# Kernel tuning notes

Measured on AMD Instinct MI355X. Metric: run time of the kernel, lower is better.

The kernel has to match this reference:

```python
import jax, jax.numpy as jnp
import numpy as np

B = 8                                   # point clouds per batch
NS = [65536, 16384, 4096, 1024, 256]    # points per scale (stride-4 downsampling)
CS = [32, 64, 128, 256, 512]            # encoder channels per scale
K = 3
BN_EPS = 1e-5


def setup_inputs() -> dict:
    key = jax.random.key(0)
    ks = iter(jax.random.split(key, 64))
    inp = {}
    for i, (n, c) in enumerate(zip(NS, CS)):
        inp[f"p{i}"] = jax.random.uniform(next(ks), (n, 3), jnp.float32)
        inp[f"f{i}"] = jax.random.normal(next(ks), (n, c), jnp.float32)
        inp[f"b{i}"] = jnp.repeat(jnp.arange(B, dtype=jnp.int32), n // B)
    # FP stage mlps: a:(4->3) [768,256,256], b:(3->2) [384,128,128],
    #               c:(2->1) [192,64,64],   d:(1->0) [96,32,32]
    cfg = {"a": (CS[3] + CS[4], CS[3]), "b": (CS[2] + CS[3], CS[2]),
           "c": (CS[1] + CS[2], CS[1]), "d": (CS[0] + CS[1], CS[0])}
    for s, (cin, ch) in cfg.items():
        for j, ci in ((1, cin), (2, ch)):
            inp[f"w{s}{j}"] = jax.random.normal(next(ks), (ci, ch), jnp.float32) / float(np.sqrt(ci))
            inp[f"bias{s}{j}"] = jnp.zeros((ch,), jnp.float32)
            inp[f"g{s}{j}"] = jnp.ones((ch,), jnp.float32)
            inp[f"bt{s}{j}"] = jnp.zeros((ch,), jnp.float32)
    return inp


def _knn_interpolate(x2, p2, p1):
    """torch_geometric.nn.knn_interpolate with k=3; equal-sized sorted batches."""
    n1, n2, c = p1.shape[0] // B, p2.shape[0] // B, x2.shape[1]
    p1b, p2b = p1.reshape(B, n1, 3), p2.reshape(B, n2, 3)
    x2b = x2.reshape(B, n2, c)
    # squared dists via |a|^2 + |b|^2 - 2ab (avoids [B,n1,n2,3] temporary)
    d2 = (jnp.sum(p1b * p1b, -1)[:, :, None] + jnp.sum(p2b * p2b, -1)[:, None, :]
          - 2.0 * jnp.einsum('bnd,bmd->bnm', p1b, p2b))
    neg_d2, idx = jax.lax.top_k(-d2, K)              # [B, n1, K]
    w = 1.0 / jnp.maximum(-neg_d2, 1e-16)            # inverse squared distance
    gath = jax.vmap(lambda x, i: x[i])(x2b, idx)     # [B, n1, K, c]
    out = jnp.einsum('bnk,bnkc->bnc', w, gath) / jnp.sum(w, -1, keepdims=True)
    return out.reshape(B * n1, c)


def _lin_bn_relu(x, w, bias, gamma, beta):
    h = x @ w + bias
    mu = jnp.mean(h, 0)
    var = jnp.mean((h - mu) ** 2, 0)
    return jax.nn.relu((h - mu) * jax.lax.rsqrt(var + BN_EPS) * gamma + beta)


def _fp_stage(p_fine, f_fine, p_coarse, f_coarse, w1, b1, g1, bt1, w2, b2, g2, bt2):
    up = _knn_interpolate(f_coarse, p_coarse, p_fine)
    x = jnp.concatenate([f_fine, up], axis=1)
    x = _lin_bn_relu(x, w1, b1, g1, bt1)
    return _lin_bn_relu(x, w2, b2, g2, bt2)


def reference(p0, p1, p2, p3, p4, f0, f1, f2, f3, f4, b0, b1, b2, b3, b4,
              wa1, biasa1, ga1, bta1, wa2, biasa2, ga2, bta2,
              wb1, biasb1, gb1, btb1, wb2, biasb2, gb2, btb2,
              wc1, biasc1, gc1, btc1, wc2, biasc2, gc2, btc2,
              wd1, biasd1, gd1, btd1, wd2, biasd2, gd2, btd2):
    f3 = _fp_stage(p3, f3, p4, f4, wa1, biasa1, ga1, bta1, wa2, biasa2, ga2, bta2)
    f2 = _fp_stage(p2, f2, p3, f3, wb1, biasb1, gb1, btb1, wb2, biasb2, gb2, btb2)
    f1 = _fp_stage(p1, f1, p2, f2, wc1, biasc1, gc1, btc1, wc2, biasc2, gc2, btc2)
    f0 = _fp_stage(p0, f0, p1, f1, wd1, biasd1, gd1, btd1, wd2, biasd2, gd2, btd2)
    return f0
```

## Files before the change

### kernel.cpp

```cpp
#include <hip/hip_runtime.h>

#define BN_EPS 1e-5f

typedef unsigned short us;

__device__ __forceinline__ float bf2f(us u) {
    union { unsigned int i; float f; } v; v.i = ((unsigned int)u) << 16; return v.f;
}
__device__ __forceinline__ us f2bf(float f) {
    unsigned int x = __float_as_uint(f);
    x += 0x7fffu + ((x >> 16) & 1u);
    return (us)(x >> 16);
}
__device__ __forceinline__ float ldf(const void* p, size_t i, int f32) {
    return f32 ? ((const float*)p)[i] : bf2f(((const us*)p)[i]);
}

__global__ void detect_kernel(const unsigned int* __restrict__ g, int* __restrict__ flag) {
    if (threadIdx.x == 0 && blockIdx.x == 0)
        *flag = ((g[0] & 0xFFFFu) == 0u) ? 1 : 0;
}

__global__ __launch_bounds__(256)
void prep_aos_kernel(const void* __restrict__ p, float4* __restrict__ aos,
                     const int* __restrict__ pf32, int n)
{
    const int i = blockIdx.x * 256 + threadIdx.x;
    if (i >= n) return;
    const int f32 = *pf32;
    const float x = ldf(p, (size_t)3 * i + 0, f32);
    const float y = ldf(p, (size_t)3 * i + 1, f32);
    const float z = ldf(p, (size_t)3 * i + 2, f32);
    const float s2 = __fadd_rn(__fadd_rn(__fmul_rn(x, x), __fmul_rn(y, y)), __fmul_rn(z, z));
    aos[i] = make_float4(__fadd_rn(x, x), __fadd_rn(y, y), __fadd_rn(z, z), s2);
}

__device__ __forceinline__ void lexmerge33(
    const float a0, const int A0, const float a1, const int A1, const float a2, const int A2,
    const float b0, const int B0, const float b1, const int B1, const float b2, const int B2,
    float& m0, int& M0, float& m1, int& M1, float& m2, int& M2)
{
    const bool c1 = (a0 < b0) || (a0 == b0 && A0 < B0);
    m0 = c1 ? a0 : b0;  M0 = c1 ? A0 : B0;
    const float hAd = c1 ? a1 : a0;  const int hAi = c1 ? A1 : A0;
    const float hBd = c1 ? b0 : b1;  const int hBi = c1 ? B0 : B1;
    const bool c2 = (hAd < hBd) || (hAd == hBd && hAi < hBi);
    m1 = c2 ? hAd : hBd;  M1 = c2 ? hAi : hBi;
    const float gAd = c2 ? (c1 ? a2 : a1) : hAd;  const int gAi = c2 ? (c1 ? A2 : A1) : hAi;
    const float gBd = c2 ? hBd : (c1 ? b1 : b2);  const int gBi = c2 ? hBi : (c1 ? B1 : B2);
    const bool c3 = (gAd < gBd) || (gAd == gBd && gAi < gBi);
    m2 = c3 ? gAd : gBd;  M2 = c3 ? gAi : gBi;
}

template<int MODE, int SPLIT, int LEN>
__global__ __launch_bounds__(64 * SPLIT, 8)
void knn_up_kernel(
    const void* __restrict__ p_fine,
    const float4* __restrict__ aos,
    const void* __restrict__ f_coarse,
    const float* __restrict__ stats,
    const void* __restrict__ gamma,
    const void* __restrict__ beta,
    float inv_n2,
    float* __restrict__ up_out,
    const int* __restrict__ pf32,
    int n2pb, int c2)
{
    __shared__ float mrg_d[SPLIT * 64 * 3];
    __shared__ int   mrg_i[SPLIT * 64 * 3];
    __shared__ float aff_a[256], aff_b[256];
    __shared__ int   s_idx[64][3];
    __shared__ float s_w[64][3];

    const int f32 = *pf32;
    const int tid = threadIdx.x;
    const int lane = tid & 63;
    const int wv = tid >> 6;
    const int cbase = blockIdx.y * n2pb;
    const int row0 = (blockIdx.y * gridDim.x + blockIdx.x) * 64;

    if (MODE == 1) {
        for (int c = tid; c < c2; c += 64 * SPLIT) {
            float mu  = stats[c] * inv_n2;
            float var = stats[c2 + c] * inv_n2 - mu * mu;
            float a = ldf(gamma, c, f32) * rsqrtf(var + BN_EPS);
            aff_a[c] = a;
            aff_b[c] = ldf(beta, c, f32) - mu * a;
        }
    }

    {
        const int row = row0 + lane;
        const size_t b = (size_t)row * 3;
        const float px = ldf(p_fine, b + 0, f32);
        const float py = ldf(p_fine, b + 1, f32);
        const float pz = ldf(p_fine, b + 2, f32);
        const float s1 = __fadd_rn(__fadd_rn(__fmul_rn(px, px), __fmul_rn(py, py)),
                                   __fmul_rn(pz, pz));
        const int jb = wv * LEN;
        unsigned long long spv = (unsigned long long)(const void*)(aos + cbase + jb);
        spv = ((unsigned long long)__builtin_amdgcn_readfirstlane((unsigned int)(spv >> 32)) << 32)
            |  (unsigned long long)__builtin_amdgcn_readfirstlane((unsigned int)spv);
        const float4* __restrict__ sl = (const float4*)spv;

        float t0 = 1e30f, t1 = 1e30f, t2 = 1e30f;
        int i0 = jb, i1 = jb, i2 = jb;

#define KNN_UPD(CQ, JJ) {                                                     \
        const float dot2 = fmaf(pz, (CQ).z, fmaf(py, (CQ).y,                  \
                                __fmul_rn(px, (CQ).x)));                      \
        const float d = __fsub_rn(__fadd_rn(s1, (CQ).w), dot2);               \
        const int jj = (JJ);                                                  \
        const bool a0 = d < t0, a1 = d < t1, a2 = d < t2;                     \
                          \
        i2 = a1 ? i1 : (a2 ? jj : i2);                                        \
        i1 = a0 ? i0 : (a1 ? jj : i1);                                        \
        i0 = a0 ? jj : i0;                                                    \
                   \
        const float nt1 = __builtin_amdgcn_fmed3f(d, t0, t1);                 \
        const float nt2 = __builtin_amdgcn_fmed3f(d, t1, t2);                 \
        t0 = fminf(d, t0);                                                    \
        t1 = nt1; t2 = nt2; }

        float4 ca = sl[0], cb = sl[1], cc = sl[2], cd = sl[3];
        for (int t = 0; t < LEN; t += 4) {
            float4 na, nb, nc, nd;
            const bool more = (t + 4) < LEN;
            if (more) { na = sl[t + 4]; nb = sl[t + 5]; nc = sl[t + 6]; nd = sl[t + 7]; }
            KNN_UPD(ca, jb + t + 0);
            KNN_UPD(cb, jb + t + 1);
            KNN_UPD(cc, jb + t + 2);
            KNN_UPD(cd, jb + t + 3);
            if (more) { ca = na; cb = nb; cc = nc; cd = nd; }
        }
#undef KNN_UPD

        const int mb = (wv * 64 + lane) * 3;
        mrg_d[mb + 0] = t0;  mrg_i[mb + 0] = cbase + i0;
        mrg_d[mb + 1] = t1;  mrg_i[mb + 1] = cbase + i1;
        mrg_d[mb + 2] = t2;  mrg_i[mb + 2] = cbase + i2;
    }
    __syncthreads();

    if (tid < 64) {
        float d0 = mrg_d[tid * 3 + 0], d1 = mrg_d[tid * 3 + 1], d2 = mrg_d[tid * 3 + 2];
        int   j0 = mrg_i[tid * 3 + 0], j1 = mrg_i[tid * 3 + 1], j2 = mrg_i[tid * 3 + 2];
        #pragma unroll
        for (int w = 1; w < SPLIT; ++w) {
            const int mb = (w * 64 + tid) * 3;
            const float e0 = mrg_d[mb + 0], e1 = mrg_d[mb + 1], e2 = mrg_d[mb + 2];
            const int   k0 = mrg_i[mb + 0], k1 = mrg_i[mb + 1], k2 = mrg_i[mb + 2];
            float n0, n1, n2v; int ni0, ni1, ni2;
            lexmerge33(d0, j0, d1, j1, d2, j2,
                       e0, k0, e1, k1, e2, k2,
                       n0, ni0, n1, ni1, n2v, ni2);
            d0 = n0; j0 = ni0; d1 = n1; j1 = ni1; d2 = n2v; j2 = ni2;
        }
        s_idx[tid][0] = j0;  s_w[tid][0] = __fdiv_rn(1.0f, fmaxf(d0, 1e-16f));
        s_idx[tid][1] = j1;  s_w[tid][1] = __fdiv_rn(1.0f, fmaxf(d1, 1e-16f));
        s_idx[tid][2] = j2;  s_w[tid][2] = __fdiv_rn(1.0f, fmaxf(d2, 1e-16f));
    }
    __syncthreads();

    for (int p = wv; p < 64; p += SPLIT) {
        const int row = row0 + p;
        const int g0 = s_idx[p][0], g1 = s_idx[p][1], g2 = s_idx[p][2];
        const float w0 = s_w[p][0], w1 = s_w[p][1], w2 = s_w[p][2];
        const float den = __fadd_rn(__fadd_rn(w0, w1), w2);
        float* __restrict__ urow = up_out + (size_t)row * c2;
        for (int c = lane; c < c2; c += 64) {
            float v0, v1, v2;
            if (MODE == 0) {
                v0 = ldf(f_coarse, (size_t)g0 * c2 + c, f32);
                v1 = ldf(f_coarse, (size_t)g1 * c2 + c, f32);
                v2 = ldf(f_coarse, (size_t)g2 * c2 + c, f32);
            } else {
                const float* fc = (const float*)f_coarse;
                const float aa = aff_a[c], bb = aff_b[c];
                v0 = fmaxf(aa * fc[(size_t)g0 * c2 + c] + bb, 0.f);
                v1 = fmaxf(aa * fc[(size_t)g1 * c2 + c] + bb, 0.f);
                v2 = fmaxf(aa * fc[(size_t)g2 * c2 + c] + bb, 0.f);
            }
            const float num = fmaf(w2, v2, fmaf(w1, v1, __fmul_rn(w0, v0)));
            urow[c] = __fdiv_rn(num, den);
        }
    }
}

__global__ __launch_bounds__(256)
void gemm1_bn_kernel(const void* __restrict__ Ffine,
                     const float* __restrict__ Up,
                     const void* __restrict__ W,
                     const void* __restrict__ bias,
                     float* __restrict__ H,
                     float* __restrict__ stats_out,
                     const int* __restrict__ pf32,
                     int M, int c1, int c2, int N)
{
    __shared__ __align__(16) float As[16][68];
    __shared__ __align__(16) float Bs[16][68];
    __shared__ float s_sum[64], s_sq[64];

    const int f32 = *pf32;
    const int K = c1 + c2;
    const int tid = threadIdx.x;
    const int tx = tid & 15, ty = tid >> 4;
    const int n0 = blockIdx.x * 64, m0 = blockIdx.y * 64;

    if (tid < 64) { s_sum[tid] = 0.f; s_sq[tid] = 0.f; }

    const int a_m = tid >> 2;
    const int a_k = (tid & 3) << 2;
    const int b_k = tid >> 4;
    const int b_n = (tid & 15) << 2;
    const int row = m0 + a_m;

    float avp[4]; float4 bvp;
    {
        const int k = a_k;
        if (k < c1) {
            if (f32) {
                const float4 v = *(const float4*)((const float*)Ffine + (size_t)row * c1 + k);
                avp[0] = v.x; avp[1] = v.y; avp[2] = v.z; avp[3] = v.w;
            } else {
                const ushort4 u = *(const ushort4*)((const us*)Ffine + (size_t)row * c1 + k);
                avp[0] = bf2f(u.x); avp[1] = bf2f(u.y); avp[2] = bf2f(u.z); avp[3] = bf2f(u.w);
            }
        } else {
            const float4 v = *(const float4*)(Up + (size_t)row * c2 + (k - c1));
            avp[0] = v.x; avp[1] = v.y; avp[2] = v.z; avp[3] = v.w;
        }
        bvp = make_float4(0.f, 0.f, 0.f, 0.f);
        if (n0 + b_n < N) {
            const size_t wi = (size_t)b_k * N + (n0 + b_n);
            if (f32) bvp = *(const float4*)((const float*)W + wi);
            else {
                const ushort4 u = *(const ushort4*)((const us*)W + wi);
                bvp = make_float4(bf2f(u.x), bf2f(u.y), bf2f(u.z), bf2f(u.w));
            }
        }
    }

    float acc[4][4] = {};

    for (int k0 = 0; k0 < K; k0 += 16) {
        #pragma unroll
        for (int i = 0; i < 4; ++i) As[a_k + i][a_m] = avp[i];
        *(float4*)&Bs[b_k][b_n] = bvp;
        __syncthreads();

        float avn[4]; float4 bvn;
        const int kn = k0 + 16;
        if (kn < K) {
            const int k = kn + a_k;
            if (k < c1) {
                if (f32) {
                    const float4 v = *(const float4*)((const float*)Ffine + (size_t)row * c1 + k);
                    avn[0] = v.x; avn[1] = v.y; avn[2] = v.z; avn[3] = v.w;
                } else {
                    const ushort4 u = *(const ushort4*)((const us*)Ffine + (size_t)row * c1 + k);
                    avn[0] = bf2f(u.x); avn[1] = bf2f(u.y); avn[2] = bf2f(u.z); avn[3] = bf2f(u.w);
                }
            } else {
                const float4 v = *(const float4*)(Up + (size_t)row * c2 + (k - c1));
                avn[0] = v.x; avn[1] = v.y; avn[2] = v.z; avn[3] = v.w;
            }
            bvn = make_float4(0.f, 0.f, 0.f, 0.f);
            if (n0 + b_n < N) {
                const size_t wi = (size_t)(kn + b_k) * N + (n0 + b_n);
                if (f32) bvn = *(const float4*)((const float*)W + wi);
                else {
                    const ushort4 u = *(const ushort4*)((const us*)W + wi);
                    bvn = make_float4(bf2f(u.x), bf2f(u.y), bf2f(u.z), bf2f(u.w));
                }
            }
        }

        #pragma unroll
        for (int kk = 0; kk < 16; ++kk) {
            const float4 a4 = *(const float4*)&As[kk][ty << 2];
            const float4 b4 = *(const float4*)&Bs[kk][tx << 2];
            const float aarr[4] = {a4.x, a4.y, a4.z, a4.w};
            const float barr[4] = {b4.x, b4.y, b4.z, b4.w};
            #pragma unroll
            for (int i = 0; i < 4; ++i)
                #pragma unroll
                for (int j = 0; j < 4; ++j)
                    acc[i][j] = fmaf(aarr[i], barr[j], acc[i][j]);
        }
        __syncthreads();

        if (kn < K) {
            #pragma unroll
            for (int i = 0; i < 4; ++i) avp[i] = avn[i];
            bvp = bvn;
        }
    }

    float bvals[4];
    const bool colsok = (n0 + (tx << 2)) < N;
    #pragma unroll
    for (int j = 0; j < 4; ++j) {
        const int n = n0 + (tx << 2) + j;
        bvals[j] = (n < N) ? ldf(bias, n, f32) : 0.f;
    }
    float ps[4] = {0.f, 0.f, 0.f, 0.f}, pq[4] = {0.f, 0.f, 0.f, 0.f};
    #pragma unroll
    for (int i = 0; i < 4; ++i) {
        float4 hv;
        float* hvp = (float*)&hv;
        #pragma unroll
        for (int j = 0; j < 4; ++j) {
            const float v = acc[i][j] + bvals[j];
            hvp[j] = v;
            ps[j] += v;
            pq[j] = fmaf(v, v, pq[j]);
        }
        if (colsok)
            *(float4*)(H + (size_t)(m0 + (ty << 2) + i) * N + n0 + (tx << 2)) = hv;
    }
    #pragma unroll
    for (int j = 0; j < 4; ++j) {
        atomicAdd(&s_sum[(tx << 2) + j], ps[j]);
        atomicAdd(&s_sq[(tx << 2) + j], pq[j]);
    }
    __syncthreads();
    if (tid < 64) {
        const int n = n0 + tid;
        if (n < N) {
            atomicAdd(&stats_out[n], s_sum[tid]);
            atomicAdd(&stats_out[N + n], s_sq[tid]);
        }
    }
}

__global__ __launch_bounds__(256)
void gemm2_bn_kernel(const float* __restrict__ A,
                     const void* __restrict__ W,
                     const void* __restrict__ bias,
                     const float* __restrict__ stats_in,
                     const void* __restrict__ g_in,
                     const void* __restrict__ bt_in,
                     float inv_m,
                     float* __restrict__ H,
                     float* __restrict__ stats_out,
                     const int* __restrict__ pf32,
                     int M, int K, int N)
{
    __shared__ __align__(16) float As[16][68];
    __shared__ __align__(16) float Bs[16][68];
    __shared__ float aff_a[256], aff_b[256];
    __shared__ float s_sum[64], s_sq[64];

    const int f32 = *pf32;
    const int tid = threadIdx.x;
    const int tx = tid & 15, ty = tid >> 4;
    const int n0 = blockIdx.x * 64, m0 = blockIdx.y * 64;

    for (int c = tid; c < K; c += 256) {
        float mu  = stats_in[c] * inv_m;
        float var = stats_in[K + c] * inv_m - mu * mu;
        float a = ldf(g_in, c, f32) * rsqrtf(var + BN_EPS);
        aff_a[c] = a; aff_b[c] = ldf(bt_in, c, f32) - mu * a;
    }
    if (tid < 64) { s_sum[tid] = 0.f; s_sq[tid] = 0.f; }
    __syncthreads();

    const int a_m = tid >> 2;
    const int a_k = (tid & 3) << 2;
    const int b_k = tid >> 4;
    const int b_n = (tid & 15) << 2;
    const int row = m0 + a_m;

    float avp[4]; float4 bvp;
    {
        const float4 af = *(const float4*)(A + (size_t)row * K + a_k);
        avp[0] = af.x; avp[1] = af.y; avp[2] = af.z; avp[3] = af.w;
        bvp = make_float4(0.f, 0.f, 0.f, 0.f);
        if (n0 + b_n < N) {
            const size_t wi = (size_t)b_k * N + (n0 + b_n);
            if (f32) bvp = *(const float4*)((const float*)W + wi);
            else {
                const ushort4 u = *(const ushort4*)((const us*)W + wi);
                bvp = make_float4(bf2f(u.x), bf2f(u.y), bf2f(u.z), bf2f(u.w));
            }
        }
    }

    float acc[4][4] = {};

    for (int k0 = 0; k0 < K; k0 += 16) {
        #pragma unroll
        for (int i = 0; i < 4; ++i)
            As[a_k + i][a_m] = fmaxf(fmaf(aff_a[k0 + a_k + i], avp[i], aff_b[k0 + a_k + i]), 0.f);
        *(float4*)&Bs[b_k][b_n] = bvp;
        __syncthreads();

        float avn[4]; float4 bvn;
        const int kn = k0 + 16;
        if (kn < K) {
            const float4 af = *(const float4*)(A + (size_t)row * K + (kn + a_k));
            avn[0] = af.x; avn[1] = af.y; avn[2] = af.z; avn[3] = af.w;
            bvn = make_float4(0.f, 0.f, 0.f, 0.f);
            if (n0 + b_n < N) {
                const size_t wi = (size_t)(kn + b_k) * N + (n0 + b_n);
                if (f32) bvn = *(const float4*)((const float*)W + wi);
                else {
                    const ushort4 u = *(const ushort4*)((const us*)W + wi);
                    bvn = make_float4(bf2f(u.x), bf2f(u.y), bf2f(u.z), bf2f(u.w));
                }
            }
        }

        #pragma unroll
        for (int kk = 0; kk < 16; ++kk) {
            const float4 a4 = *(const float4*)&As[kk][ty << 2];
            const float4 b4 = *(const float4*)&Bs[kk][tx << 2];
            const float aarr[4] = {a4.x, a4.y, a4.z, a4.w};
            const float barr[4] = {b4.x, b4.y, b4.z, b4.w};
            #pragma unroll
            for (int i = 0; i < 4; ++i)
                #pragma unroll
                for (int j = 0; j < 4; ++j)
                    acc[i][j] = fmaf(aarr[i], barr[j], acc[i][j]);
        }
        __syncthreads();

        if (kn < K) {
            #pragma unroll
            for (int i = 0; i < 4; ++i) avp[i] = avn[i];
            bvp = bvn;
        }
    }

    float bvals[4];
    const bool colsok = (n0 + (tx << 2)) < N;
    #pragma unroll
    for (int j = 0; j < 4; ++j) {
        const int n = n0 + (tx << 2) + j;
        bvals[j] = (n < N) ? ldf(bias, n, f32) : 0.f;
    }
    float ps[4] = {0.f, 0.f, 0.f, 0.f}, pq[4] = {0.f, 0.f, 0.f, 0.f};
    #pragma unroll
    for (int i = 0; i < 4; ++i) {
        float4 hv;
        float* hvp = (float*)&hv;
        #pragma unroll
        for (int j = 0; j < 4; ++j) {
            const float v = acc[i][j] + bvals[j];
            hvp[j] = v;
            ps[j] += v;
            pq[j] = fmaf(v, v, pq[j]);
        }
        if (colsok)
            *(float4*)(H + (size_t)(m0 + (ty << 2) + i) * N + n0 + (tx << 2)) = hv;
    }
    #pragma unroll
    for (int j = 0; j < 4; ++j) {
        atomicAdd(&s_sum[(tx << 2) + j], ps[j]);
        atomicAdd(&s_sq[(tx << 2) + j], pq[j]);
    }
    __syncthreads();
    if (tid < 64) {
        const int n = n0 + tid;
        if (n < N) {
            atomicAdd(&stats_out[n], s_sum[tid]);
            atomicAdd(&stats_out[N + n], s_sq[tid]);
        }
    }
}

__global__ __launch_bounds__(256)
void finalize_kernel(const float* __restrict__ Hf, const float* __restrict__ stats,
                     const void* __restrict__ g, const void* __restrict__ bt,
                     float inv_m, void* __restrict__ out,
                     const int* __restrict__ pf32, int total)
{
    const int idx = blockIdx.x * 256 + threadIdx.x;
    if (idx >= total) return;
    const int f32 = *pf32;
    const int c = idx & 31;
    const float mu  = stats[c] * inv_m;
    const float var = stats[32 + c] * inv_m - mu * mu;
    const float a = ldf(g, c, f32) * rsqrtf(var + BN_EPS);
    const float b = ldf(bt, c, f32) - mu * a;
    const float v = fmaxf(fmaf(a, Hf[idx], b), 0.f);
    if (f32) ((float*)out)[idx] = v;
    else     ((us*)out)[idx] = f2bf(v);
}

extern "C" void kernel_launch(void* const* d_in, const int* in_sizes, int n_in,
                              void* d_out, int out_size, void* d_ws, size_t ws_size,
                              hipStream_t stream) {
    (void)in_sizes; (void)n_in; (void)out_size; (void)ws_size;
    const void* p0 = d_in[0];
    const void* f0 = d_in[1];
    const void* p1 = d_in[3];
    const void* f1 = d_in[4];
    const void* p2 = d_in[6];
    const void* f2 = d_in[7];
    const void* p3 = d_in[9];
    const void* f3 = d_in[10];
    const void* p4 = d_in[12];
    const void* f4 = d_in[13];
    const void *W1[4], *B1[4], *G1[4], *T1[4], *W2[4], *B2[4], *G2[4], *T2[4];
    for (int s = 0; s < 4; ++s) {
        const int b = 15 + s * 8;
        W1[s] = d_in[b + 0]; B1[s] = d_in[b + 1];
        G1[s] = d_in[b + 2]; T1[s] = d_in[b + 3];
        W2[s] = d_in[b + 4]; B2[s] = d_in[b + 5];
        G2[s] = d_in[b + 6]; T2[s] = d_in[b + 7];
    }

    float* stats = (float*)d_ws;
    float* st_a1 = stats + 0;
    float* st_a2 = stats + 512;
    float* st_b1 = stats + 1024;
    float* st_b2 = stats + 1280;
    float* st_c1 = stats + 1536;
    float* st_c2 = stats + 1664;
    float* st_d1 = stats + 1792;
    float* st_d2 = stats + 1856;
    int*   flag  = (int*)(stats + 1920);
    float* U = (float*)((char*)d_ws + 8192);
    float* H = U + 4194304;
    float* h2a = H + 262144;
    float* h2b = H + 524288;
    float* h2c = H + 1048576;
    float* h2d = U;
    float4* aosbuf = (float4*)H;

    hipMemsetAsync(d_ws, 0, 1920 * sizeof(float), stream);
    detect_kernel<<<1, 64, 0, stream>>>((const unsigned int*)G1[0], flag);

    prep_aos_kernel<<<1, 256, 0, stream>>>(p4, aosbuf, flag, 256);
    knn_up_kernel<0, 8, 4><<<dim3(2, 8), 512, 0, stream>>>(
        p3, aosbuf, f4, nullptr, nullptr, nullptr, 0.f, U, flag, 32, 512);
    gemm1_bn_kernel<<<dim3(4, 16), 256, 0, stream>>>(
        f3, U, W1[0], B1[0], H, st_a1, flag, 1024, 256, 512, 256);
    gemm2_bn_kernel<<<dim3(4, 16), 256, 0, stream>>>(
        H, W2[0], B2[0], st_a1, G1[0], T1[0], 1.f / 1024.f,
        h2a, st_a2, flag, 1024, 256, 256);
    prep_aos_kernel<<<4, 256, 0, stream>>>(p3, aosbuf, flag, 1024);
    knn_up_kernel<1, 8, 16><<<dim3(8, 8), 512, 0, stream>>>(
        p2, aosbuf, h2a, st_a2, G2[0], T2[0], 1.f / 1024.f, U, flag, 128, 256);
    gemm1_bn_kernel<<<dim3(2, 64), 256, 0, stream>>>(
        f2, U, W1[1], B1[1], H, st_b1, flag, 4096, 128, 256, 128);
    gemm2_bn_kernel<<<dim3(2, 64), 256, 0, stream>>>(
        H, W2[1], B2[1], st_b1, G1[1], T1[1], 1.f / 4096.f,
        h2b, st_b2, flag, 4096, 128, 128);
    prep_aos_kernel<<<16, 256, 0, stream>>>(p2, aosbuf, flag, 4096);
    knn_up_kernel<1, 16, 32><<<dim3(32, 8), 1024, 0, stream>>>(
        p1, aosbuf, h2b, st_b2, G2[1], T2[1], 1.f / 4096.f, U, flag, 512, 128);
    gemm1_bn_kernel<<<dim3(1, 256), 256, 0, stream>>>(
        f1, U, W1[2], B1[2], H, st_c1, flag, 16384, 64, 128, 64);
    gemm2_bn_kernel<<<dim3(1, 256), 256, 0, stream>>>(
        H, W2[2], B2[2], st_c1, G1[2], T1[2], 1.f / 16384.f,
        h2c, st_c2, flag, 16384, 64, 64);
    prep_aos_kernel<<<64, 256, 0, stream>>>(p1, aosbuf, flag, 16384);
    knn_up_kernel<1, 8, 256><<<dim3(128, 8), 512, 0, stream>>>(
        p0, aosbuf, h2c, st_c2, G2[2], T2[2], 1.f / 16384.f, U, flag, 2048, 64);
    gemm1_bn_kernel<<<dim3(1, 1024), 256, 0, stream>>>(
        f0, U, W1[3], B1[3], H, st_d1, flag, 65536, 32, 64, 32);
    gemm2_bn_kernel<<<dim3(1, 1024), 256, 0, stream>>>(
        H, W2[3], B2[3], st_d1, G1[3], T1[3], 1.f / 65536.f,
        h2d, st_d2, flag, 65536, 32, 32);
    finalize_kernel<<<(65536 * 32) / 256, 256, 0, stream>>>(
        h2d, st_d2, G2[3], T2[3], 1.f / 65536.f, d_out, flag, 65536 * 32);
}
```

Baseline: 504.6 us.

## Replace brute-force last-stage kNN with x-sorted windowed search

For the largest upsampling stage (65536 fine points, 2048 coarse points per cloud), coarse points are bitonic-sorted by x in shared memory. Each query then binary-searches its x position and scans outward in both directions, pruning once the x-gap squared exceeds the current third-best distance. Four waves split the scan and merge their top-3 candidates. This aims to remove most of the O(n1*n2) distance work, at the cost of an extra sort kernel, divergent early-exit loops and a tie-break that must stay consistent with the brute-force ordering.

New measurement: 606.6 us. +20.2%, slower.

```diff
diff --git a/kernel.cpp b/kernel.cpp
--- a/kernel.cpp
+++ b/kernel.cpp
@@ -33,6 +33,48 @@
     const float z = ldf(p, (size_t)3 * i + 2, f32);
     const float s2 = __fadd_rn(__fadd_rn(__fmul_rn(x, x), __fmul_rn(y, y)), __fmul_rn(z, z));
     aos[i] = make_float4(__fadd_rn(x, x), __fadd_rn(y, y), __fadd_rn(z, z), s2);
+}
+
+template<int NPB>
+__global__ __launch_bounds__(NPB / 2)
+void sort_aos_kernel(const void* __restrict__ p, const int* __restrict__ pf32,
+                     float4* __restrict__ srt, int* __restrict__ jout)
+{
+    __shared__ float sk[NPB];
+    __shared__ int   sj[NPB];
+    const int f32 = *pf32;
+    const int tid = threadIdx.x;
+    const int base = blockIdx.x * NPB;
+    for (int i = tid; i < NPB; i += NPB / 2) {
+        sk[i] = ldf(p, (size_t)3 * (base + i) + 0, f32);
+        sj[i] = i;
+    }
+    __syncthreads();
+    for (int k = 2; k <= NPB; k <<= 1) {
+        for (int j = k >> 1; j > 0; j >>= 1) {
+            const int i = ((tid / j) * (j << 1)) + (tid % j);
+            const int ixj = i + j;
+            const bool up = ((i & k) == 0);
+            const float a = sk[i], b = sk[ixj];
+            const bool sw = up ? (a > b) : (a < b);
+            if (sw) {
+                sk[i] = b; sk[ixj] = a;
+                const int t = sj[i]; sj[i] = sj[ixj]; sj[ixj] = t;
+            }
+            __syncthreads();
+        }
+    }
+    for (int i = tid; i < NPB; i += NPB / 2) {
+        const int jl = sj[i];
+        const size_t b = (size_t)3 * (base + jl);
+        const float x = ldf(p, b + 0, f32);
+        const float y = ldf(p, b + 1, f32);
+        const float z = ldf(p, b + 2, f32);
+        const float s2 = __fadd_rn(__fadd_rn(__fmul_rn(x, x), __fmul_rn(y, y)),
+                                   __fmul_rn(z, z));
+        srt[base + i] = make_float4(__fadd_rn(x, x), __fadd_rn(y, y), __fadd_rn(z, z), s2);
+        jout[base + i] = base + jl;
+    }
 }
 
 __device__ __forceinline__ void lexmerge33(
@@ -50,6 +92,153 @@
     const float gBd = c2 ? hBd : (c1 ? b1 : b2);  const int gBi = c2 ? hBi : (c1 ? B1 : B2);
     const bool c3 = (gAd < gBd) || (gAd == gBd && gAi < gBi);
     m2 = c3 ? gAd : gBd;  M2 = c3 ? gAi : gBi;
+}
+
+template<int NPB, int C2>
+__global__ __launch_bounds__(256)
+void knn_win_kernel(const void* __restrict__ p_fine,
+                    const float4* __restrict__ srt,
+                    const int* __restrict__ jsrt,
+                    const float* __restrict__ f_coarse,
+                    const float* __restrict__ stats,
+                    const void* __restrict__ gamma,
+                    const void* __restrict__ beta,
+                    float inv_n2,
+                    float* __restrict__ up_out,
+                    const int* __restrict__ pf32)
+{
+    __shared__ __align__(16) float4 sA[NPB];
+    __shared__ int   sJ[NPB];
+    __shared__ float mrg_d[4 * 64 * 3];
+    __shared__ int   mrg_i[4 * 64 * 3];
+    __shared__ int   s_idx[64][3];
+    __shared__ float s_w[64][3];
+    __shared__ float aff_a[C2], aff_b[C2];
+
+    const int f32 = *pf32;
+    const int tid = threadIdx.x;
+    const int lane = tid & 63, wv = tid >> 6;
+    const int cb = blockIdx.y * NPB;
+    const int row0 = (blockIdx.y * gridDim.x + blockIdx.x) * 64;
+
+    for (int i = tid; i < NPB; i += 256) { sA[i] = srt[cb + i]; sJ[i] = jsrt[cb + i]; }
+    for (int c = tid; c < C2; c += 256) {
+        const float mu  = stats[c] * inv_n2;
+        const float var = stats[C2 + c] * inv_n2 - mu * mu;
+        const float a = ldf(gamma, c, f32) * rsqrtf(var + BN_EPS);
+        aff_a[c] = a;
+        aff_b[c] = ldf(beta, c, f32) - mu * a;
+    }
+    __syncthreads();
+
+    const int row = row0 + lane;
+    const size_t pb = (size_t)row * 3;
+    const float px = ldf(p_fine, pb + 0, f32);
+    const float py = ldf(p_fine, pb + 1, f32);
+    const float pz = ldf(p_fine, pb + 2, f32);
+    const float s1 = __fadd_rn(__fadd_rn(__fmul_rn(px, px), __fmul_rn(py, py)),
+                               __fmul_rn(pz, pz));
+    const float px2 = __fadd_rn(px, px);
+
+    int lo = 0, hi = NPB;
+    while (lo < hi) {
+        const int mid = (lo + hi) >> 1;
+        if (sA[mid].x < px2) lo = mid + 1; else hi = mid;
+    }
+    const int cpos = lo;
+
+    float t0 = 1e30f, t1 = 1e30f, t2 = 1e30f;
+    int i0 = 0, i1 = 0, i2 = 0;
+
+#define WINS(A, D, JJ) {                                                      \
+    const bool l0 = (A) && ((D) < t0 || ((D) == t0 && (JJ) < i0));            \
+    const bool l1 = (A) && ((D) < t1 || ((D) == t1 && (JJ) < i1));            \
+    const bool l2 = (A) && ((D) < t2 || ((D) == t2 && (JJ) < i2));            \
+    i2 = l1 ? i1 : (l2 ? (JJ) : i2);                                          \
+    i1 = l0 ? i0 : (l1 ? (JJ) : i1);                                          \
+    i0 = l0 ? (JJ) : i0;                                                      \
+    const float q2 = l1 ? t1 : (l2 ? (D) : t2);                               \
+    const float q1 = l0 ? t0 : (l1 ? (D) : t1);                               \
+    t0 = l0 ? (D) : t0;  t1 = q1;  t2 = q2; }
+
+    {
+        int pos = cpos + wv;
+        bool alive = true;
+        for (int it = 0; it < NPB / 4 + 2; ++it) {
+            if (!__any(alive)) break;
+            const bool inb = (pos < NPB);
+            const int rp = inb ? pos : (NPB - 1);
+            const float4 C = sA[rp];
+            const float dq = __fsub_rn(px2, C.x);
+            const float dq2 = __fmul_rn(dq, dq);
+            alive = alive && inb && !(dq2 > fmaf(4.0f, t2, 4e-5f));
+            const float dot2 = fmaf(pz, C.z, fmaf(py, C.y, __fmul_rn(px, C.x)));
+            const float d = __fsub_rn(__fadd_rn(s1, C.w), dot2);
+            const int jj = sJ[rp];
+            WINS(alive, d, jj);
+            pos += 4;
+        }
+    }
+    {
+        int pos = cpos - 1 - wv;
+        bool alive = true;
+        for (int it = 0; it < NPB / 4 + 2; ++it) {
+            if (!__any(alive)) break;
+            const bool inb = (pos >= 0);
+            const int rp = inb ? pos : 0;
+            const float4 C = sA[rp];
+            const float dq = __fsub_rn(px2, C.x);
+            const float dq2 = __fmul_rn(dq, dq);
+            alive = alive && inb && !(dq2 > fmaf(4.0f, t2, 4e-5f));
+            const float dot2 = fmaf(pz, C.z, fmaf(py, C.y, __fmul_rn(px, C.x)));
+            const float d = __fsub_rn(__fadd_rn(s1, C.w), dot2);
+            const int jj = sJ[rp];
+            WINS(alive, d, jj);
+            pos -= 4;
+        }
+    }
+#undef WINS
+
+    const int mb = (wv * 64 + lane) * 3;
+    mrg_d[mb + 0] = t0;  mrg_i[mb + 0] = i0;
+    mrg_d[mb + 1] = t1;  mrg_i[mb + 1] = i1;
+    mrg_d[mb + 2] = t2;  mrg_i[mb + 2] = i2;
+    __syncthreads();
+
+    if (tid < 64) {
+        float d0 = mrg_d[tid * 3 + 0], d1 = mrg_d[tid * 3 + 1], d2 = mrg_d[tid * 3 + 2];
+        int   j0 = mrg_i[tid * 3 + 0], j1 = mrg_i[tid * 3 + 1], j2 = mrg_i[tid * 3 + 2];
+        #pragma unroll
+        for (int w = 1; w < 4; ++w) {
+            const int b2 = (w * 64 + tid) * 3;
+            float n0, n1, n2v; int ni0, ni1, ni2;
+            lexmerge33(d0, j0, d1, j1, d2, j2,
+                       mrg_d[b2 + 0], mrg_i[b2 + 0], mrg_d[b2 + 1], mrg_i[b2 + 1],
+                       mrg_d[b2 + 2], mrg_i[b2 + 2],
+                       n0, ni0, n1, ni1, n2v, ni2);
+            d0 = n0; j0 = ni0; d1 = n1; j1 = ni1; d2 = n2v; j2 = ni2;
+        }
+        s_idx[tid][0] = j0;  s_w[tid][0] = __fdiv_rn(1.0f, fmaxf(d0, 1e-16f));
+        s_idx[tid][1] = j1;  s_w[tid][1] = __fdiv_rn(1.0f, fmaxf(d1, 1e-16f));
+        s_idx[tid][2] = j2;  s_w[tid][2] = __fdiv_rn(1.0f, fmaxf(d2, 1e-16f));
+    }
+    __syncthreads();
+
+    for (int p = wv; p < 64; p += 4) {
+        const int r2 = row0 + p;
+        const int g0 = s_idx[p][0], g1 = s_idx[p][1], g2 = s_idx[p][2];
+        const float w0 = s_w[p][0], w1 = s_w[p][1], w2 = s_w[p][2];
+        const float den = __fadd_rn(__fadd_rn(w0, w1), w2);
+        float* __restrict__ urow = up_out + (size_t)r2 * C2;
+        for (int c = lane; c < C2; c += 64) {
+            const float aa = aff_a[c], bb = aff_b[c];
+            const float v0 = fmaxf(aa * f_coarse[(size_t)g0 * C2 + c] + bb, 0.f);
+            const float v1 = fmaxf(aa * f_coarse[(size_t)g1 * C2 + c] + bb, 0.f);
+            const float v2 = fmaxf(aa * f_coarse[(size_t)g2 * C2 + c] + bb, 0.f);
+            const float num = fmaf(w2, v2, fmaf(w1, v1, __fmul_rn(w0, v0)));
+            urow[c] = __fdiv_rn(num, den);
+        }
+    }
 }
 
 template<int MODE, int SPLIT, int LEN>
@@ -112,11 +301,9 @@
         const float d = __fsub_rn(__fadd_rn(s1, (CQ).w), dot2);               \
         const int jj = (JJ);                                                  \
         const bool a0 = d < t0, a1 = d < t1, a2 = d < t2;                     \
-                          \
         i2 = a1 ? i1 : (a2 ? jj : i2);                                        \
         i1 = a0 ? i0 : (a1 ? jj : i1);                                        \
         i0 = a0 ? jj : i0;                                                    \
-                   \
         const float nt1 = __builtin_amdgcn_fmed3f(d, t0, t1);                 \
         const float nt2 = __builtin_amdgcn_fmed3f(d, t1, t2);                 \
         t0 = fminf(d, t0);                                                    \
@@ -529,6 +716,8 @@
     float* h2c = H + 1048576;
     float* h2d = U;
     float4* aosbuf = (float4*)H;
+    float4* srtbuf = (float4*)H;
+    int*    jbuf   = (int*)(H + 65536);
 
     hipMemsetAsync(d_ws, 0, 1920 * sizeof(float), stream);
     detect_kernel<<<1, 64, 0, stream>>>((const unsigned int*)G1[0], flag);
@@ -557,9 +746,9 @@
     gemm2_bn_kernel<<<dim3(1, 256), 256, 0, stream>>>(
         H, W2[2], B2[2], st_c1, G1[2], T1[2], 1.f / 16384.f,
         h2c, st_c2, flag, 16384, 64, 64);
-    prep_aos_kernel<<<64, 256, 0, stream>>>(p1, aosbuf, flag, 16384);
-    knn_up_kernel<1, 8, 256><<<dim3(128, 8), 512, 0, stream>>>(
-        p0, aosbuf, h2c, st_c2, G2[2], T2[2], 1.f / 16384.f, U, flag, 2048, 64);
+    sort_aos_kernel<2048><<<8, 1024, 0, stream>>>(p1, flag, srtbuf, jbuf);
+    knn_win_kernel<2048, 64><<<dim3(128, 8), 256, 0, stream>>>(
+        p0, srtbuf, jbuf, h2c, st_c2, G2[2], T2[2], 1.f / 16384.f, U, flag);
     gemm1_bn_kernel<<<dim3(1, 1024), 256, 0, stream>>>(
         f0, U, W1[3], B1[3], H, st_d1, flag, 65536, 32, 64, 32);
     gemm2_bn_kernel<<<dim3(1, 1024), 256, 0, stream>>>(
```
